# Kernel tuning notes

Measured on AMD Instinct MI355X. Metric: run time of the kernel, lower is better.

The kernel has to match this reference:

```python
import jax, jax.numpy as jnp
import numpy as np

NUM_BBOX = 2
NUM_CLASSES = 20
NUM_GRID = 7
THR_CONF = 0.5
THR_NMS = 0.3
BATCH = 64


def setup_inputs() -> dict:
    key = jax.random.key(0)
    pyolos = jax.random.uniform(key, (BATCH, NUM_GRID, NUM_GRID, NUM_BBOX * (5 + NUM_CLASSES)), dtype=jnp.float32)
    return {"pyolos": pyolos}


def _decode(pyolos):
    # pyolos: [B, R, C, nb*(5+nc)]
    B, R, C, D = pyolos.shape
    p = pyolos.reshape(B, R, C, NUM_BBOX, 5 + NUM_CLASSES)
    # score per bbox = conf * max class prob  -> [B,R,C,nb]
    scores_all = jnp.max(p[..., 5:] * p[..., 4:5], axis=-1)
    # per-cell best bbox (original gathers pyolos_max over the bbox dim)
    best = jnp.argmax(scores_all, axis=-1)                              # [B,R,C]
    pmax = jnp.take_along_axis(p, best[..., None, None], axis=3)[:, :, :, 0, :]  # [B,R,C,5+nc]
    labels = (jnp.argmax(pmax[..., 5:], axis=-1) + 1).astype(jnp.float32)        # [B,R,C]
    # offxy2xy: colrow_index = [row, col] exactly as in the original loop
    rows = jnp.arange(R, dtype=pyolos.dtype)[None, :, None]
    cols = jnp.arange(C, dtype=pyolos.dtype)[None, None, :]
    x = (pmax[..., 0] + rows) / NUM_GRID
    y = (pmax[..., 1] + cols) / NUM_GRID
    w = pmax[..., 2]
    h = pmax[..., 3]
    half_w = w * 0.5
    half_h = h * 0.5
    ltrb = jnp.stack([x - half_w, y - half_h, x + half_w, y + half_h], axis=-1)  # [B,R,C,4]
    N = B * R * C * NUM_BBOX
    # each (cell, bbox) candidate shares the cell's best-bbox box/label, has its own score
    boxes = jnp.broadcast_to(ltrb[:, :, :, None, :], (B, R, C, NUM_BBOX, 4)).reshape(N, 4)
    labs = jnp.broadcast_to(labels[:, :, :, None], (B, R, C, NUM_BBOX)).reshape(N)
    bids = jnp.broadcast_to(jnp.arange(B, dtype=jnp.float32)[:, None, None, None], (B, R, C, NUM_BBOX)).reshape(N)
    scores = scores_all.reshape(N)
    valid = scores > THR_CONF
    return boxes, labs, bids, scores, valid


def _label_nms(boxes, labels, bids, scores, valid):
    N = scores.shape[0]
    # sort by score descending, invalid candidates last
    order = jnp.argsort(jnp.where(valid, -scores, jnp.inf))
    b = boxes[order]
    l = labels[order]
    ib = bids[order]
    s = scores[order]
    v = valid[order]
    # pairwise IoU  [N,N]
    lt = jnp.maximum(b[:, None, :2], b[None, :, :2])
    rb = jnp.minimum(b[:, None, 2:], b[None, :, 2:])
    wh = jnp.clip(rb - lt, 0.0)
    inter = wh[..., 0] * wh[..., 1]
    area = (b[:, 2] - b[:, 0]) * (b[:, 3] - b[:, 1])
    iou = inter / (area[:, None] + area[None, :] - inter + 1e-9)
    same = (l[:, None] == l[None, :]) & (ib[:, None] == ib[None, :])
    later = jnp.arange(N)[None, :] > jnp.arange(N)[:, None]
    sup = (iou > THR_NMS) & same & later  # sup[i,j]: i suppresses later j

    def body(i, keep):
        return keep & ~(keep[i] & sup[i])

    keep = jax.lax.fori_loop(0, N, body, v)
    return ib, b, l, s, keep


def reference(pyolos):
    boxes, labels, bids, scores, valid = _decode(pyolos)
    ids_batch, p_boxes_ltrb, p_labels, p_scores, keep = _label_nms(boxes, labels, bids, scores, valid)
    # fixed-shape analogue of the dynamic outputs: keep mask marks surviving detections
    return ids_batch, p_boxes_ltrb, p_labels, p_scores, keep
```

## Files before the change

### kernel.cpp

```cpp
#include <hip/hip_runtime.h>
#include <stdint.h>

#define NUM_BBOX    2
#define NUM_CLASSES 20
#define NUM_GRID    7
#define BATCH       64
#define NCELL  (BATCH * NUM_GRID * NUM_GRID)
#define NCAND  (NCELL * NUM_BBOX)
#define NGROUP (BATCH * NUM_CLASSES)
#define MAXG   98
#define CPB    49
#define KPB    98
#define NJT    8
#define JTILE  (NCAND / NJT)
#define JCELLS (JTILE / 2)

#define NDECB   49
#define B_RANK0 NDECB
#define B_NMS0  (NDECB + 784)
#define NBLK_K1 (NDECB + 784 + NGROUP)

#define WS_SCORE     0
#define WS_CELLBOX   25088
#define WS_CELLLAB   75264
#define WS_KEEP      87808
#define WS_RANKP     112896

__device__ __forceinline__ unsigned fkey(float f) {
    unsigned u = __float_as_uint(f);
    return (u & 0x80000000u) ? ~u : (u | 0x80000000u);
}

__device__ __forceinline__ float cand_score(const float* q) {
    float conf = q[4];
    float m = __fmul_rn(q[5], conf);
    #pragma unroll
    for (int k = 1; k < NUM_CLASSES; ++k)
        m = fmaxf(m, __fmul_rn(q[5 + k], conf));
    return m;
}

__device__ __forceinline__ float iou_rn(float4 a, float4 b) {
    float xx1 = fmaxf(a.x, b.x), yy1 = fmaxf(a.y, b.y);
    float xx2 = fminf(a.z, b.z), yy2 = fminf(a.w, b.w);
    float w = fmaxf(__fsub_rn(xx2, xx1), 0.0f);
    float h = fmaxf(__fsub_rn(yy2, yy1), 0.0f);
    float inter = __fmul_rn(w, h);
    float aa = __fmul_rn(__fsub_rn(a.z, a.x), __fsub_rn(a.w, a.y));
    float ab = __fmul_rn(__fsub_rn(b.z, b.x), __fsub_rn(b.w, b.y));
    float denom = __fadd_rn(__fsub_rn(__fadd_rn(aa, ab), inter), 1e-9f);
    return __fdiv_rn(inter, denom);
}

__global__ void __launch_bounds__(64) k_main(
        const float* __restrict__ in,
        float* __restrict__ score,
        float* __restrict__ cellBox,
        float* __restrict__ cellLabel,
        float* __restrict__ keepOrig,
        unsigned* __restrict__ rankPart) {
    __shared__ union SMem {
        unsigned long long jkey[JTILE];
        struct {
            float2 raw2[1225];
            unsigned long long lkey[KPB];
            float4 lbox[CPB];
            int    llab[CPB];
            float  lkeep[KPB];
            unsigned long long mkey[KPB];
            unsigned long long skey[KPB];
        } nms;
    } sm;

    const int bid  = (int)blockIdx.x;
    const int lane = (int)threadIdx.x;

    if (bid < NDECB) {
        int cell = bid * 64 + lane;
        const float* p = in + cell * 50;
        float s0 = cand_score(p);
        float s1 = cand_score(p + 25);
        int best = (s1 > s0) ? 1 : 0;
        const float* q = p + best * 25;

        int lab = 0; float bv = q[5];
        #pragma unroll
        for (int k = 1; k < NUM_CLASSES; ++k)
            if (q[5 + k] > bv) { bv = q[5 + k]; lab = k; }

        int rc = cell % (NUM_GRID * NUM_GRID);
        int r = rc / NUM_GRID, c = rc % NUM_GRID;
        float x  = __fdiv_rn(__fadd_rn(q[0], (float)r), 7.0f);
        float y  = __fdiv_rn(__fadd_rn(q[1], (float)c), 7.0f);
        float hw = __fmul_rn(q[2], 0.5f);
        float hh = __fmul_rn(q[3], 0.5f);
        *(float4*)(cellBox + cell * 4) =
            make_float4(__fsub_rn(x, hw), __fsub_rn(y, hh),
                        __fadd_rn(x, hw), __fadd_rn(y, hh));
        cellLabel[cell] = (float)(lab + 1);
        score[cell * 2 + 0] = s0;
        score[cell * 2 + 1] = s1;
        return;
    }

    if (bid < B_NMS0) {
        int rb = bid - B_RANK0;
        int ib = rb >> 3;
        int jt = rb & 7;

        for (int cl = lane; cl < JCELLS; cl += 64) {
            int cell = jt * JCELLS + cl;
            const float* p = in + cell * 50;
            #pragma unroll
            for (int bb = 0; bb < 2; ++bb) {
                float s = cand_score(p + bb * 25);
                bool valid = s > 0.5f;
                float kf = valid ? -s : __builtin_inff();
                sm.jkey[cl * 2 + bb] =
                    ((unsigned long long)fkey(kf) << 32) | (unsigned)(cell * 2 + bb);
            }
        }
        int i = ib * 64 + lane;
        unsigned long long my;
        {
            const float* q = in + (i >> 1) * 50 + (i & 1) * 25;
            float s = cand_score(q);
            bool valid = s > 0.5f;
            float kf = valid ? -s : __builtin_inff();
            my = ((unsigned long long)fkey(kf) << 32) | (unsigned)i;
        }
        __syncthreads();

        unsigned r = 0;
        #pragma unroll 8
        for (int j = 0; j < JTILE; ++j)
            r += (sm.jkey[j] < my) ? 1u : 0u;
        rankPart[jt * NCAND + i] = r;
        return;
    }

    int g = bid - B_NMS0;
    int b = g / NUM_CLASSES;
    int L = g % NUM_CLASSES + 1;
    int base = b * KPB;

    const float2* src = (const float2*)(in + b * (CPB * 50));
    for (int t = lane; t < 1225; t += 64) sm.nms.raw2[t] = src[t];
    sm.nms.lkeep[lane] = 0.0f;
    if (lane + 64 < KPB) sm.nms.lkeep[lane + 64] = 0.0f;
    __syncthreads();

    if (lane < CPB) {
        const float* p = (const float*)sm.nms.raw2 + lane * 50;
        float s0 = cand_score(p);
        float s1 = cand_score(p + 25);
        int best = (s1 > s0) ? 1 : 0;
        const float* q = p + best * 25;

        int lab = 0; float bv = q[5];
        #pragma unroll
        for (int k = 1; k < NUM_CLASSES; ++k)
            if (q[5 + k] > bv) { bv = q[5 + k]; lab = k; }

        int r = lane / NUM_GRID, c = lane % NUM_GRID;
        float x  = __fdiv_rn(__fadd_rn(q[0], (float)r), 7.0f);
        float y  = __fdiv_rn(__fadd_rn(q[1], (float)c), 7.0f);
        float hw = __fmul_rn(q[2], 0.5f);
        float hh = __fmul_rn(q[3], 0.5f);
        sm.nms.lbox[lane] = make_float4(__fsub_rn(x, hw), __fsub_rn(y, hh),
                                        __fadd_rn(x, hw), __fadd_rn(y, hh));
        sm.nms.llab[lane] = lab + 1;
        float ss0 = s0, ss1 = s1;
        {
            bool valid = ss0 > 0.5f;
            float kf = valid ? -ss0 : __builtin_inff();
            sm.nms.lkey[lane * 2 + 0] =
                ((unsigned long long)fkey(kf) << 32) | (unsigned)(base + lane * 2 + 0);
        }
        {
            bool valid = ss1 > 0.5f;
            float kf = valid ? -ss1 : __builtin_inff();
            sm.nms.lkey[lane * 2 + 1] =
                ((unsigned long long)fkey(kf) << 32) | (unsigned)(base + lane * 2 + 1);
        }
    }
    __syncthreads();

    unsigned long long key0 = sm.nms.lkey[lane];
    int lab0 = sm.nms.llab[lane >> 1];
    bool v0 = ((unsigned)(key0 >> 32) < 0x80000000u) && (lab0 == L);
    unsigned long long key1 = 0; bool v1 = false; int lab1 = -1;
    if (lane + 64 < KPB) {
        key1 = sm.nms.lkey[lane + 64];
        lab1 = sm.nms.llab[(lane + 64) >> 1];
        v1 = ((unsigned)(key1 >> 32) < 0x80000000u) && (lab1 == L);
    }
    unsigned long long b0 = __ballot(v0);
    unsigned long long b1 = __ballot(v1);
    int n0 = __popcll(b0);
    int n  = n0 + __popcll(b1);
    unsigned long long below = (1ull << lane) - 1ull;
    if (v0) sm.nms.mkey[__popcll(b0 & below)] = key0;
    if (v1) sm.nms.mkey[n0 + __popcll(b1 & below)] = key1;
    __syncthreads();

    if (n > 0) {
        for (int s = 0; s < 2; ++s) {
            int j = lane + s * 64;
            if (j < n) {
                unsigned long long kj = sm.nms.mkey[j];
                int rr = 0;
                for (int i2 = 0; i2 < n; ++i2) rr += (sm.nms.mkey[i2] < kj) ? 1 : 0;
                sm.nms.skey[rr] = kj;
            }
        }
    }
    __syncthreads();

    if (n > 0) {
        float4 box0 = make_float4(0.f, 0.f, 0.f, 0.f), box1 = box0;
        int t0 = 0, t1 = 0, keep0 = 0, keep1 = 0;
        if (lane < n) {
            t0 = (int)(unsigned)sm.nms.skey[lane] - base;
            box0 = sm.nms.lbox[t0 >> 1];
            keep0 = 1;
        }
        if (lane + 64 < n) {
            t1 = (int)(unsigned)sm.nms.skey[lane + 64] - base;
            box1 = sm.nms.lbox[t1 >> 1];
            keep1 = 1;
        }
        for (int i = 0; i < n; ++i) {
            int srcl = i & 63;
            int ki = __shfl((i < 64) ? keep0 : keep1, srcl);
            if (ki) {
                float4 s4 = (i < 64) ? box0 : box1;
                float4 bi;
                bi.x = __shfl(s4.x, srcl);
                bi.y = __shfl(s4.y, srcl);
                bi.z = __shfl(s4.z, srcl);
                bi.w = __shfl(s4.w, srcl);
                if (keep0 && lane > i)      { if (iou_rn(bi, box0) > 0.3f) keep0 = 0; }
                if (keep1 && lane + 64 > i) { if (iou_rn(bi, box1) > 0.3f) keep1 = 0; }
            }
        }
        if (keep0) sm.nms.lkeep[t0] = 1.0f;
        if (keep1) sm.nms.lkeep[t1] = 1.0f;
    }
    __syncthreads();

    if (lab0 == L) keepOrig[base + lane] = sm.nms.lkeep[lane];
    if (lane + 64 < KPB && lab1 == L) keepOrig[base + lane + 64] = sm.nms.lkeep[lane + 64];
}

__global__ void __launch_bounds__(64) k_scatter(
        const unsigned* __restrict__ rankPart,
        const float* __restrict__ score,
        const float* __restrict__ cellBox,
        const float* __restrict__ cellLabel,
        const float* __restrict__ keepOrig,
        float* __restrict__ out) {
    int i = blockIdx.x * 64 + (int)threadIdx.x;
    unsigned r = 0;
    #pragma unroll
    for (int jt = 0; jt < NJT; ++jt) r += rankPart[jt * NCAND + i];
    int cell = i >> 1;
    out[r] = (float)(i / 98);
    float4 bx = *(const float4*)(cellBox + cell * 4);
    *(float4*)(out + NCAND + r * 4) = bx;
    out[NCAND * 5 + r] = cellLabel[cell];
    out[NCAND * 6 + r] = score[i];
    out[NCAND * 7 + r] = keepOrig[i];
}

extern "C" void kernel_launch(void* const* d_in, const int* in_sizes, int n_in,
                              void* d_out, int out_size, void* d_ws, size_t ws_size,
                              hipStream_t stream) {
    const float* in = (const float*)d_in[0];
    char* ws = (char*)d_ws;
    float*    score     = (float*)(ws + WS_SCORE);
    float*    cellBox   = (float*)(ws + WS_CELLBOX);
    float*    cellLabel = (float*)(ws + WS_CELLLAB);
    float*    keepOrig  = (float*)(ws + WS_KEEP);
    unsigned* rankPart  = (unsigned*)(ws + WS_RANKP);
    float* out = (float*)d_out;

    k_main<<<NBLK_K1, 64, 0, stream>>>(in, score, cellBox, cellLabel, keepOrig, rankPart);
    k_scatter<<<NCAND / 64, 64, 0, stream>>>(rankPart, score, cellBox, cellLabel,
                                             keepOrig, out);
}
```

Before: 23.41 us.

## Move global rank computation into scatter kernel using compacted valid-key counting

Removes the 784 rank blocks from the first kernel; the decode blocks now emit 32-bit sort keys. The scatter kernel uses 512 threads per block to compact only the valid keys into shared memory, counts ranks against that compacted list split across 8 waves, and places invalid candidates by closed-form index arithmetic. This cuts redundant score recomputation and the O(N^2) comparisons over invalid candidates. In exchange, every block repeats the full key load and compaction, and the rank step now sits after the decode/NMS kernel instead of running alongside it.

New measurement: 27.33 us. +16.8%, slower.

```diff
diff --git a/kernel.cpp b/kernel.cpp
--- a/kernel.cpp
+++ b/kernel.cpp
@@ -1,30 +1,25 @@
 #include <hip/hip_runtime.h>
 #include <stdint.h>
 
-#define NUM_BBOX    2
 #define NUM_CLASSES 20
 #define NUM_GRID    7
-#define BATCH       64
-#define NCELL  (BATCH * NUM_GRID * NUM_GRID)
-#define NCAND  (NCELL * NUM_BBOX)
-#define NGROUP (BATCH * NUM_CLASSES)
-#define MAXG   98
-#define CPB    49
-#define KPB    98
-#define NJT    8
-#define JTILE  (NCAND / NJT)
-#define JCELLS (JTILE / 2)
-
+#define BATCH   64
+#define NCELL   3136
+#define NCAND   6272
+#define NGROUP  1280
+#define CPB     49
+#define KPB     98
 #define NDECB   49
-#define B_RANK0 NDECB
-#define B_NMS0  (NDECB + 784)
-#define NBLK_K1 (NDECB + 784 + NGROUP)
+#define NBLK_K1 (NDECB + NGROUP)
+#define NW      8
+#define TPB2    512
+#define NCHUNK  98
 
 #define WS_SCORE     0
 #define WS_CELLBOX   25088
 #define WS_CELLLAB   75264
-#define WS_KEEP      87808
-#define WS_RANKP     112896
+#define WS_KEYLO     87808
+#define WS_KEEP      112896
 
 __device__ __forceinline__ unsigned fkey(float f) {
     unsigned u = __float_as_uint(f);
@@ -52,24 +47,21 @@
     return __fdiv_rn(inter, denom);
 }
 
-__global__ void __launch_bounds__(64) k_main(
+__global__ void __launch_bounds__(64) k_decode_nms(
         const float* __restrict__ in,
         float* __restrict__ score,
         float* __restrict__ cellBox,
         float* __restrict__ cellLabel,
-        float* __restrict__ keepOrig,
-        unsigned* __restrict__ rankPart) {
-    __shared__ union SMem {
-        unsigned long long jkey[JTILE];
-        struct {
-            float2 raw2[1225];
-            unsigned long long lkey[KPB];
-            float4 lbox[CPB];
-            int    llab[CPB];
-            float  lkeep[KPB];
-            unsigned long long mkey[KPB];
-            unsigned long long skey[KPB];
-        } nms;
+        unsigned* __restrict__ keyLo,
+        float* __restrict__ keepOrig) {
+    __shared__ struct {
+        float2 raw2[1225];
+        unsigned long long lkey[KPB];
+        float4 lbox[CPB];
+        int    llab[CPB];
+        float  lkeep[KPB];
+        unsigned long long mkey[KPB];
+        unsigned long long skey[KPB];
     } sm;
 
     const int bid  = (int)blockIdx.x;
@@ -100,58 +92,24 @@
         cellLabel[cell] = (float)(lab + 1);
         score[cell * 2 + 0] = s0;
         score[cell * 2 + 1] = s1;
+        keyLo[cell * 2 + 0] = fkey((s0 > 0.5f) ? -s0 : __builtin_inff());
+        keyLo[cell * 2 + 1] = fkey((s1 > 0.5f) ? -s1 : __builtin_inff());
         return;
     }
 
-    if (bid < B_NMS0) {
-        int rb = bid - B_RANK0;
-        int ib = rb >> 3;
-        int jt = rb & 7;
-
-        for (int cl = lane; cl < JCELLS; cl += 64) {
-            int cell = jt * JCELLS + cl;
-            const float* p = in + cell * 50;
-            #pragma unroll
-            for (int bb = 0; bb < 2; ++bb) {
-                float s = cand_score(p + bb * 25);
-                bool valid = s > 0.5f;
-                float kf = valid ? -s : __builtin_inff();
-                sm.jkey[cl * 2 + bb] =
-                    ((unsigned long long)fkey(kf) << 32) | (unsigned)(cell * 2 + bb);
-            }
-        }
-        int i = ib * 64 + lane;
-        unsigned long long my;
-        {
-            const float* q = in + (i >> 1) * 50 + (i & 1) * 25;
-            float s = cand_score(q);
-            bool valid = s > 0.5f;
-            float kf = valid ? -s : __builtin_inff();
-            my = ((unsigned long long)fkey(kf) << 32) | (unsigned)i;
-        }
-        __syncthreads();
-
-        unsigned r = 0;
-        #pragma unroll 8
-        for (int j = 0; j < JTILE; ++j)
-            r += (sm.jkey[j] < my) ? 1u : 0u;
-        rankPart[jt * NCAND + i] = r;
-        return;
-    }
-
-    int g = bid - B_NMS0;
+    int g = bid - NDECB;
     int b = g / NUM_CLASSES;
     int L = g % NUM_CLASSES + 1;
     int base = b * KPB;
 
     const float2* src = (const float2*)(in + b * (CPB * 50));
-    for (int t = lane; t < 1225; t += 64) sm.nms.raw2[t] = src[t];
-    sm.nms.lkeep[lane] = 0.0f;
-    if (lane + 64 < KPB) sm.nms.lkeep[lane + 64] = 0.0f;
+    for (int t = lane; t < 1225; t += 64) sm.raw2[t] = src[t];
+    sm.lkeep[lane] = 0.0f;
+    if (lane + 64 < KPB) sm.lkeep[lane + 64] = 0.0f;
     __syncthreads();
 
     if (lane < CPB) {
-        const float* p = (const float*)sm.nms.raw2 + lane * 50;
+        const float* p = (const float*)sm.raw2 + lane * 50;
         float s0 = cand_score(p);
         float s1 = cand_score(p + 25);
         int best = (s1 > s0) ? 1 : 0;
@@ -167,32 +125,31 @@
         float y  = __fdiv_rn(__fadd_rn(q[1], (float)c), 7.0f);
         float hw = __fmul_rn(q[2], 0.5f);
         float hh = __fmul_rn(q[3], 0.5f);
-        sm.nms.lbox[lane] = make_float4(__fsub_rn(x, hw), __fsub_rn(y, hh),
-                                        __fadd_rn(x, hw), __fadd_rn(y, hh));
-        sm.nms.llab[lane] = lab + 1;
-        float ss0 = s0, ss1 = s1;
+        sm.lbox[lane] = make_float4(__fsub_rn(x, hw), __fsub_rn(y, hh),
+                                    __fadd_rn(x, hw), __fadd_rn(y, hh));
+        sm.llab[lane] = lab + 1;
         {
-            bool valid = ss0 > 0.5f;
-            float kf = valid ? -ss0 : __builtin_inff();
-            sm.nms.lkey[lane * 2 + 0] =
-                ((unsigned long long)fkey(kf) << 32) | (unsigned)(base + lane * 2 + 0);
+            bool v = s0 > 0.5f;
+            float kf = v ? -s0 : __builtin_inff();
+            sm.lkey[lane * 2] =
+                ((unsigned long long)fkey(kf) << 32) | (unsigned)(base + lane * 2);
         }
         {
-            bool valid = ss1 > 0.5f;
-            float kf = valid ? -ss1 : __builtin_inff();
-            sm.nms.lkey[lane * 2 + 1] =
+            bool v = s1 > 0.5f;
+            float kf = v ? -s1 : __builtin_inff();
+            sm.lkey[lane * 2 + 1] =
                 ((unsigned long long)fkey(kf) << 32) | (unsigned)(base + lane * 2 + 1);
         }
     }
     __syncthreads();
 
-    unsigned long long key0 = sm.nms.lkey[lane];
-    int lab0 = sm.nms.llab[lane >> 1];
+    unsigned long long key0 = sm.lkey[lane];
+    int lab0 = sm.llab[lane >> 1];
     bool v0 = ((unsigned)(key0 >> 32) < 0x80000000u) && (lab0 == L);
     unsigned long long key1 = 0; bool v1 = false; int lab1 = -1;
     if (lane + 64 < KPB) {
-        key1 = sm.nms.lkey[lane + 64];
-        lab1 = sm.nms.llab[(lane + 64) >> 1];
+        key1 = sm.lkey[lane + 64];
+        lab1 = sm.llab[(lane + 64) >> 1];
         v1 = ((unsigned)(key1 >> 32) < 0x80000000u) && (lab1 == L);
     }
     unsigned long long b0 = __ballot(v0);
@@ -200,18 +157,18 @@
     int n0 = __popcll(b0);
     int n  = n0 + __popcll(b1);
     unsigned long long below = (1ull << lane) - 1ull;
-    if (v0) sm.nms.mkey[__popcll(b0 & below)] = key0;
-    if (v1) sm.nms.mkey[n0 + __popcll(b1 & below)] = key1;
+    if (v0) sm.mkey[__popcll(b0 & below)] = key0;
+    if (v1) sm.mkey[n0 + __popcll(b1 & below)] = key1;
     __syncthreads();
 
     if (n > 0) {
         for (int s = 0; s < 2; ++s) {
             int j = lane + s * 64;
             if (j < n) {
-                unsigned long long kj = sm.nms.mkey[j];
+                unsigned long long kj = sm.mkey[j];
                 int rr = 0;
-                for (int i2 = 0; i2 < n; ++i2) rr += (sm.nms.mkey[i2] < kj) ? 1 : 0;
-                sm.nms.skey[rr] = kj;
+                for (int i2 = 0; i2 < n; ++i2) rr += (sm.mkey[i2] < kj) ? 1 : 0;
+                sm.skey[rr] = kj;
             }
         }
     }
@@ -221,14 +178,12 @@
         float4 box0 = make_float4(0.f, 0.f, 0.f, 0.f), box1 = box0;
         int t0 = 0, t1 = 0, keep0 = 0, keep1 = 0;
         if (lane < n) {
-            t0 = (int)(unsigned)sm.nms.skey[lane] - base;
-            box0 = sm.nms.lbox[t0 >> 1];
-            keep0 = 1;
+            t0 = (int)(unsigned)sm.skey[lane] - base;
+            box0 = sm.lbox[t0 >> 1]; keep0 = 1;
         }
         if (lane + 64 < n) {
-            t1 = (int)(unsigned)sm.nms.skey[lane + 64] - base;
-            box1 = sm.nms.lbox[t1 >> 1];
-            keep1 = 1;
+            t1 = (int)(unsigned)sm.skey[lane + 64] - base;
+            box1 = sm.lbox[t1 >> 1]; keep1 = 1;
         }
         for (int i = 0; i < n; ++i) {
             int srcl = i & 63;
@@ -236,41 +191,112 @@
             if (ki) {
                 float4 s4 = (i < 64) ? box0 : box1;
                 float4 bi;
-                bi.x = __shfl(s4.x, srcl);
-                bi.y = __shfl(s4.y, srcl);
-                bi.z = __shfl(s4.z, srcl);
-                bi.w = __shfl(s4.w, srcl);
+                bi.x = __shfl(s4.x, srcl); bi.y = __shfl(s4.y, srcl);
+                bi.z = __shfl(s4.z, srcl); bi.w = __shfl(s4.w, srcl);
                 if (keep0 && lane > i)      { if (iou_rn(bi, box0) > 0.3f) keep0 = 0; }
                 if (keep1 && lane + 64 > i) { if (iou_rn(bi, box1) > 0.3f) keep1 = 0; }
             }
         }
-        if (keep0) sm.nms.lkeep[t0] = 1.0f;
-        if (keep1) sm.nms.lkeep[t1] = 1.0f;
-    }
-    __syncthreads();
-
-    if (lab0 == L) keepOrig[base + lane] = sm.nms.lkeep[lane];
-    if (lane + 64 < KPB && lab1 == L) keepOrig[base + lane + 64] = sm.nms.lkeep[lane + 64];
-}
-
-__global__ void __launch_bounds__(64) k_scatter(
-        const unsigned* __restrict__ rankPart,
+        if (keep0) sm.lkeep[t0] = 1.0f;
+        if (keep1) sm.lkeep[t1] = 1.0f;
+    }
+    __syncthreads();
+
+    if (lab0 == L) keepOrig[base + lane] = sm.lkeep[lane];
+    if (lane + 64 < KPB && lab1 == L) keepOrig[base + lane + 64] = sm.lkeep[lane + 64];
+}
+
+__global__ void __launch_bounds__(TPB2) k_rank_scatter(
+        const unsigned* __restrict__ keyLo,
         const float* __restrict__ score,
         const float* __restrict__ cellBox,
         const float* __restrict__ cellLabel,
         const float* __restrict__ keepOrig,
         float* __restrict__ out) {
-    int i = blockIdx.x * 64 + (int)threadIdx.x;
-    unsigned r = 0;
+    __shared__ unsigned vkey[NCAND];
+    __shared__ unsigned chunkCnt[NCHUNK];
+    __shared__ unsigned chunkOff[NCHUNK];
+    __shared__ unsigned prefVOwn[64];
+    __shared__ unsigned rankPart[NW][64];
+    __shared__ unsigned nV_s;
+
+    const int tid  = (int)threadIdx.x;
+    const int lane = tid & 63;
+    const int w    = tid >> 6;
+    const int ib   = (int)blockIdx.x;
+    const int i0   = ib * 64;
+
+    unsigned kreg[13];
     #pragma unroll
-    for (int jt = 0; jt < NJT; ++jt) r += rankPart[jt * NCAND + i];
-    int cell = i >> 1;
-    out[r] = (float)(i / 98);
-    float4 bx = *(const float4*)(cellBox + cell * 4);
-    *(float4*)(out + NCAND + r * 4) = bx;
-    out[NCAND * 5 + r] = cellLabel[cell];
-    out[NCAND * 6 + r] = score[i];
-    out[NCAND * 7 + r] = keepOrig[i];
+    for (int k = 0; k < 13; ++k) {
+        int ch = NW * k + w;
+        kreg[k] = (ch < NCHUNK) ? keyLo[ch * 64 + lane] : 0xFFFFFFFFu;
+    }
+    #pragma unroll
+    for (int k = 0; k < 13; ++k) {
+        int ch = NW * k + w;
+        if (ch < NCHUNK) {
+            unsigned long long bal = __ballot(kreg[k] < 0x80000000u);
+            if (lane == 0) chunkCnt[ch] = (unsigned)__popcll(bal);
+        }
+    }
+    __syncthreads();
+    if (tid < NCHUNK) {
+        unsigned off = 0;
+        for (int t = 0; t < tid; ++t) off += chunkCnt[t];
+        chunkOff[tid] = off;
+        if (tid == NCHUNK - 1) nV_s = off + chunkCnt[NCHUNK - 1];
+    }
+    __syncthreads();
+    #pragma unroll
+    for (int k = 0; k < 13; ++k) {
+        int ch = NW * k + w;
+        if (ch < NCHUNK) {
+            bool val = kreg[k] < 0x80000000u;
+            unsigned long long bal = __ballot(val);
+            unsigned pos = chunkOff[ch] +
+                (unsigned)__popcll(bal & ((1ull << lane) - 1ull));
+            if (val) vkey[pos] = kreg[k];
+            if (ch == ib) prefVOwn[lane] = pos;
+        }
+    }
+    __syncthreads();
+
+    const int iG = i0 + lane;
+    unsigned kiLo = keyLo[iG];
+    unsigned ci   = prefVOwn[lane];
+    {
+        unsigned nV = nV_s;
+        int cs = ((int)nV + NW - 1) / NW;
+        int j0 = w * cs;
+        int j1 = min((int)nV, j0 + cs);
+        unsigned acc = 0;
+        #pragma unroll 8
+        for (int j = j0; j < j1; ++j) {
+            unsigned kj = vkey[j];
+            acc += (kj < kiLo) ? 1u : 0u;
+            acc += (kj == kiLo && (unsigned)j < ci) ? 1u : 0u;
+        }
+        rankPart[w][lane] = acc;
+    }
+    __syncthreads();
+    if (tid < 64) {
+        unsigned r;
+        if (kiLo < 0x80000000u) {
+            r = 0;
+            #pragma unroll
+            for (int w2 = 0; w2 < NW; ++w2) r += rankPart[w2][lane];
+        } else {
+            r = nV_s + (unsigned)iG - ci;
+        }
+        int cell = iG >> 1;
+        out[r] = (float)(iG / KPB);
+        float4 bx = *(const float4*)(cellBox + cell * 4);
+        *(float4*)(out + NCAND + r * 4) = bx;
+        out[NCAND * 5 + r] = cellLabel[cell];
+        out[NCAND * 6 + r] = score[iG];
+        out[NCAND * 7 + r] = keepOrig[iG];
+    }
 }
 
 extern "C" void kernel_launch(void* const* d_in, const int* in_sizes, int n_in,
@@ -281,11 +307,12 @@
     float*    score     = (float*)(ws + WS_SCORE);
     float*    cellBox   = (float*)(ws + WS_CELLBOX);
     float*    cellLabel = (float*)(ws + WS_CELLLAB);
+    unsigned* keyLo     = (unsigned*)(ws + WS_KEYLO);
     float*    keepOrig  = (float*)(ws + WS_KEEP);
-    unsigned* rankPart  = (unsigned*)(ws + WS_RANKP);
     float* out = (float*)d_out;
 
-    k_main<<<NBLK_K1, 64, 0, stream>>>(in, score, cellBox, cellLabel, keepOrig, rankPart);
-    k_scatter<<<NCAND / 64, 64, 0, stream>>>(rankPart, score, cellBox, cellLabel,
-                                             keepOrig, out);
-}
+    k_decode_nms<<<NBLK_K1, 64, 0, stream>>>(in, score, cellBox, cellLabel,
+                                             keyLo, keepOrig);
+    k_rank_scatter<<<NCHUNK, TPB2, 0, stream>>>(keyLo, score, cellBox, cellLabel,
+                                                keepOrig, out);
+}
```
